# Performance work log

Hardware: AMD Instinct MI355X
Metric: run time of the kernel (lower is better)

## Reference

```python
import jax, jax.numpy as jnp
import numpy as np

B, L, D, H = 4, 2048, 1024, 16
DV = D // H


def setup_inputs() -> dict:
    key = jax.random.key(0)
    ks = jax.random.split(key, 11)
    s = 1.0 / np.sqrt(D)
    return {
        "query": jax.random.normal(ks[0], (B, L, D), jnp.float32),
        "key": jax.random.normal(ks[1], (B, L, D), jnp.float32),
        "value": jax.random.normal(ks[2], (B, L, D), jnp.float32),
        "Wq": jax.random.normal(ks[3], (D, D), jnp.float32) * s,
        "bq": jnp.zeros((D,), jnp.float32),
        "Wk": jax.random.normal(ks[4], (D, D), jnp.float32) * s,
        "bk": jnp.zeros((D,), jnp.float32),
        "Wv": jax.random.normal(ks[5], (D, D), jnp.float32) * s,
        "bv": jnp.zeros((D,), jnp.float32),
        "Wc": jax.random.normal(ks[6], (D, D), jnp.float32) * s,
        "bc": jnp.zeros((D,), jnp.float32),
    }


def _split(x):
    # [B, L, D] -> [B, H, L, DV]
    b, l, d = x.shape
    return x.reshape(b, l, H, DV).transpose(0, 2, 1, 3)


def reference(query, key, value, Wq, bq, Wk, bk, Wv, bv, Wc, bc):
    # Linear projections (torch Linear: x @ W.T + b)
    hq = _split(query @ Wq.T + bq)
    hk = _split(key @ Wk.T + bk)
    hv = _split(value @ Wv.T + bv)
    scale = 1.0 / jnp.sqrt(jnp.float32(DV))
    scores = jnp.einsum("bhqd,bhkd->bhqk", hq, hk) * scale  # [B,H,L,L]
    p = jax.nn.softmax(scores, axis=-1)
    out = jnp.einsum("bhqk,bhkd->bhqd", p, hv)  # [B,H,L,DV]
    out = out.transpose(0, 2, 1, 3).reshape(out.shape[0], out.shape[2], D)
    return out @ Wc.T + bc
```

## Files before the change

kernel.cpp:

```cpp
#include <hip/hip_runtime.h>

#define DI __device__ __forceinline__

typedef __attribute__((ext_vector_type(8))) short bf16x8;
typedef __attribute__((ext_vector_type(4))) float f32x4;
typedef __attribute__((ext_vector_type(16))) float f32x16;
typedef __attribute__((ext_vector_type(4))) unsigned u32x4;
typedef __attribute__((ext_vector_type(2))) unsigned u32x2;

static constexpr int B_ = 4, L_ = 2048, D_ = 1024, H_ = 16, DV_ = 64;
static constexpr int M_ = B_ * L_;
static constexpr float SCALE_LOG2 = 0.18033688011112042f;

DI short f2b(float f) {
  union { float f; unsigned u; } v; v.f = f;
  unsigned r = v.u + 0x7FFFu + ((v.u >> 16) & 1u);
  return (short)(r >> 16);
}

DI float b2f(short s) {
  union { unsigned u; float f; } v;
  v.u = ((unsigned)(unsigned short)s) << 16;
  return v.f;
}

DI unsigned cvtpk(float lo, float hi) {
  unsigned r;
  asm("v_cvt_pk_bf16_f32 %0, %1, %2" : "=v"(r) : "v"(lo), "v"(hi));
  return r;
}

DI void gl_lds16(const void* g, void* l) {
  __builtin_amdgcn_global_load_lds(
      (const __attribute__((address_space(1))) unsigned int*)g,
      (__attribute__((address_space(3))) unsigned int*)l, 16, 0, 0);
}

#define MFMA16(a, b, c) __builtin_amdgcn_mfma_f32_16x16x32_bf16((a), (b), (c), 0, 0, 0)
#define MFMA32(a, b, c) __builtin_amdgcn_mfma_f32_32x32x16_bf16((a), (b), (c), 0, 0, 0)

__global__ __launch_bounds__(256) void cvtw_kernel(const float* __restrict__ W0,
                                                   const float* __restrict__ W1,
                                                   const float* __restrict__ W2,
                                                   const float* __restrict__ W3,
                                                   short* __restrict__ dst) {
  const int p = blockIdx.y;
  const float* s = p == 0 ? W0 : p == 1 ? W1 : p == 2 ? W2 : W3;
  short* d = dst + (size_t)p * 1048576;
  int i0 = (blockIdx.x * 256 + threadIdx.x) * 8;
  int stride = gridDim.x * 256 * 8;
  for (int i = i0; i < 1048576; i += stride) {
    float4 a = *(const float4*)(s + i);
    float4 b = *(const float4*)(s + i + 4);
    u32x4 o;
    o[0] = cvtpk(a.x, a.y);
    o[1] = cvtpk(a.z, a.w);
    o[2] = cvtpk(b.x, b.y);
    o[3] = cvtpk(b.z, b.w);
    *(u32x4*)(d + i) = o;
  }
}

__global__ __launch_bounds__(256) void gemm_qkvf(const float* __restrict__ Xq,
                                                 const float* __restrict__ Xk,
                                                 const float* __restrict__ Xv,
                                                 const short* __restrict__ Wall,
                                                 const float* __restrict__ bq,
                                                 const float* __restrict__ bk,
                                                 const float* __restrict__ bv,
                                                 short* __restrict__ Hq,
                                                 short* __restrict__ Hk,
                                                 short* __restrict__ Hv) {
  constexpr int K = 1024, N = 1024;
  __shared__ __align__(16) float Asf[128 * 32];
  __shared__ __align__(16) short Bs[128 * 32];
  const int p = blockIdx.y;
  const float* A = p == 0 ? Xq : p == 1 ? Xk : Xv;
  const short* Wt = Wall + (size_t)p * 1048576;
  const float* bias = p == 0 ? bq : p == 1 ? bk : bv;
  short* outb = p == 0 ? Hq : p == 1 ? Hk : Hv;

  const int tid = threadIdx.x;
  const int w = tid >> 6, lane = tid & 63;
  const int c = lane & 15, g = lane >> 4;
  const int bid = (blockIdx.x & 7) * 64 + (blockIdx.x >> 3);
  const int bn = bid & 7, bm = bid >> 3;
  const int wr = w >> 1, wc = w & 1;

  f32x4 acc[4][4] = {};

  for (int kt = 0; kt < K / 32; ++kt) {
    __syncthreads();
#pragma unroll
    for (int it = 0; it < 4; ++it) {
      int slot = it * 256 + tid;
      int row = slot >> 3, ch = (slot & 7) ^ (row & 7);
      gl_lds16(A + ((size_t)(bm * 128 + row) * K + kt * 32 + ch * 4),
               &Asf[(it * 256 + w * 64) * 4]);
    }
#pragma unroll
    for (int ia = 0; ia < 2; ++ia) {
      int slot = ia * 256 + tid;
      int row = slot >> 2, ch = slot & 3;
      gl_lds16(Wt + ((size_t)(bn * 128 + row) * K + kt * 32 + ch * 8),
               &Bs[(ia * 256 + w * 64) * 8]);
    }
    __syncthreads();
    bf16x8 af[4], bf[4];
#pragma unroll
    for (int mi = 0; mi < 4; ++mi) {
      int r = wr * 64 + mi * 16 + c;
      int c0 = (((2 * g) ^ (r & 7)) * 4);
      int c1 = (((2 * g + 1) ^ (r & 7)) * 4);
      float4 lo = *(const float4*)&Asf[r * 32 + c0];
      float4 hi = *(const float4*)&Asf[r * 32 + c1];
      u32x4 pk;
      pk[0] = cvtpk(lo.x, lo.y);
      pk[1] = cvtpk(lo.z, lo.w);
      pk[2] = cvtpk(hi.x, hi.y);
      pk[3] = cvtpk(hi.z, hi.w);
      af[mi] = __builtin_bit_cast(bf16x8, pk);
    }
#pragma unroll
    for (int ni = 0; ni < 4; ++ni)
      bf[ni] = *(const bf16x8*)&Bs[(wc * 64 + ni * 16 + c) * 32 + g * 8];
#pragma unroll
    for (int mi = 0; mi < 4; ++mi)
#pragma unroll
      for (int ni = 0; ni < 4; ++ni)
        acc[mi][ni] = MFMA16(af[mi], bf[ni], acc[mi][ni]);
  }

  float bvv[4];
#pragma unroll
  for (int ni = 0; ni < 4; ++ni) bvv[ni] = bias[bn * 128 + wc * 64 + ni * 16 + c];
#pragma unroll
  for (int mi = 0; mi < 4; ++mi)
#pragma unroll
    for (int ni = 0; ni < 4; ++ni)
#pragma unroll
      for (int j = 0; j < 4; ++j) {
        int row = bm * 128 + wr * 64 + mi * 16 + g * 4 + j;
        int col = bn * 128 + wc * 64 + ni * 16 + c;
        outb[(size_t)row * N + col] = f2b(acc[mi][ni][j] + bvv[ni]);
      }
}

template <int OUTF32>
__global__ __launch_bounds__(256) void gemm_bt(const short* __restrict__ A,
                                               const short* __restrict__ Wt,
                                               const float* __restrict__ bias,
                                               float* __restrict__ outf,
                                               short* __restrict__ outb) {
  constexpr int K = 1024, N = 1024;
  __shared__ __align__(16) short As[128 * 32];
  __shared__ __align__(16) short Bs[128 * 32];
  const int tid = threadIdx.x;
  const int w = tid >> 6, lane = tid & 63;
  const int c = lane & 15, g = lane >> 4;
  const int bid = (blockIdx.x & 7) * 64 + (blockIdx.x >> 3);
  const int bn = bid & 7, bm = bid >> 3;
  const int wr = w >> 1, wc = w & 1;

  f32x4 acc[4][4] = {};

  for (int kt = 0; kt < K / 32; ++kt) {
    __syncthreads();
#pragma unroll
    for (int ia = 0; ia < 2; ++ia) {
      int slot = ia * 256 + tid;
      int row = slot >> 2, ch = slot & 3;
      gl_lds16(A + ((size_t)(bm * 128 + row) * K + kt * 32 + ch * 8),
               &As[(ia * 256 + w * 64) * 8]);
      gl_lds16(Wt + ((size_t)(bn * 128 + row) * K + kt * 32 + ch * 8),
               &Bs[(ia * 256 + w * 64) * 8]);
    }
    __syncthreads();
    bf16x8 af[4], bf[4];
#pragma unroll
    for (int mi = 0; mi < 4; ++mi)
      af[mi] = *(const bf16x8*)&As[(wr * 64 + mi * 16 + c) * 32 + g * 8];
#pragma unroll
    for (int ni = 0; ni < 4; ++ni)
      bf[ni] = *(const bf16x8*)&Bs[(wc * 64 + ni * 16 + c) * 32 + g * 8];
#pragma unroll
    for (int mi = 0; mi < 4; ++mi)
#pragma unroll
      for (int ni = 0; ni < 4; ++ni)
        acc[mi][ni] = MFMA16(af[mi], bf[ni], acc[mi][ni]);
  }

  float bv[4];
#pragma unroll
  for (int ni = 0; ni < 4; ++ni) bv[ni] = bias[bn * 128 + wc * 64 + ni * 16 + c];
#pragma unroll
  for (int mi = 0; mi < 4; ++mi)
#pragma unroll
    for (int ni = 0; ni < 4; ++ni)
#pragma unroll
      for (int j = 0; j < 4; ++j) {
        int row = bm * 128 + wr * 64 + mi * 16 + g * 4 + j;
        int col = bn * 128 + wc * 64 + ni * 16 + c;
        float v = acc[mi][ni][j] + bv[ni];
        if (OUTF32)
          outf[(size_t)row * N + col] = v;
        else
          outb[(size_t)row * N + col] = f2b(v);
      }
}

__global__ __launch_bounds__(256) void transpose_kernel(const short* __restrict__ Hv,
                                                        short* __restrict__ Hvt) {
  __shared__ short T[64 * 72];
  int bid = blockIdx.x;
  const int lt = bid & 31;
  const int h = (bid >> 5) & 15;
  const int b = bid >> 9;
  const int l0 = lt * 64;
  const int tid = threadIdx.x;
#pragma unroll
  for (int it = 0; it < 2; ++it) {
    int slot = it * 256 + tid;
    int r = slot >> 3, ch = slot & 7;
    bf16x8 v = *(const bf16x8*)&Hv[(size_t)(b * L_ + l0 + r) * D_ + h * DV_ + ch * 8];
    *(bf16x8*)&T[r * 72 + ch * 8] = v;
  }
  __syncthreads();
#pragma unroll
  for (int it = 0; it < 2; ++it) {
    int slot = it * 256 + tid;
    int dv = slot >> 3, ch = slot & 7;
    bf16x8 o;
#pragma unroll
    for (int i = 0; i < 8; ++i) o[i] = T[(ch * 8 + i) * 72 + dv];
    *(bf16x8*)&Hvt[(size_t)((b * H_ + h) * DV_ + dv) * L_ + l0 + ch * 8] = o;
  }
}

__global__ __launch_bounds__(256, 2) void attn_kernel(const short* __restrict__ Hq,
                                                      const short* __restrict__ Hk,
                                                      const short* __restrict__ Hvt,
                                                      short* __restrict__ Aout) {
  __shared__ __align__(16) short lds[34816];
  const int tid = threadIdx.x;
  const int w = tid >> 6, lane = tid & 63;
  const int c31 = lane & 31, g1 = lane >> 5;
  const int sw = (blockIdx.x & 7) * 64 + (blockIdx.x >> 3);
  const int qb = sw & 7;
  const int h = (sw >> 3) & 15;
  const int b = sw >> 7;
  const int q0 = qb * 256;

  bf16x8 qf0[4], qf1[4];
#pragma unroll
  for (int hh = 0; hh < 2; ++hh) {
    const short* qptr =
        Hq + (size_t)(b * L_ + q0 + w * 64 + hh * 32 + c31) * D_ + h * 64 + g1 * 8;
#pragma unroll
    for (int ks = 0; ks < 4; ++ks) {
      bf16x8 raw = *(const bf16x8*)(qptr + ks * 16);
      u32x4 pk;
#pragma unroll
      for (int i = 0; i < 4; ++i)
        pk[i] = cvtpk(b2f(raw[2 * i]) * SCALE_LOG2, b2f(raw[2 * i + 1]) * SCALE_LOG2);
      if (hh == 0) qf0[ks] = __builtin_bit_cast(bf16x8, pk);
      else         qf1[ks] = __builtin_bit_cast(bf16x8, pk);
    }
  }

  f32x16 O00 = {}, O01 = {}, O10 = {}, O11 = {};
  float ls0 = 0.f, ls1 = 0.f;
  unsigned* Pw0 = (unsigned*)(lds + 16384) + (w * 2 + 0) * 1152;
  unsigned* Pw1 = (unsigned*)(lds + 16384) + (w * 2 + 1) * 1152;

  auto stage = [&](int buf, int kv0) {
    short* Kb = lds + buf * 8192;
    short* Vb = Kb + 4096;
#pragma unroll
    for (int it = 0; it < 2; ++it) {
      int slot = it * 256 + tid;
      int row = slot >> 3;
      int ch = (slot & 7) ^ (row & 7);
      gl_lds16(Hk + (size_t)(b * L_ + kv0 + row) * D_ + h * 64 + ch * 8,
               Kb + (it * 256 + w * 64) * 8);
      gl_lds16(Hvt + (size_t)((b * H_ + h) * DV_ + row) * L_ + kv0 + ch * 8,
               Vb + (it * 256 + w * 64) * 8);
    }
  };

  stage(0, 0);
  int cur = 0;
  for (int t = 0; t < L_ / 64; ++t) {
    __syncthreads();
    if (t + 1 < L_ / 64) stage(cur ^ 1, (t + 1) * 64);
    const short* Kb = lds + cur * 8192;
    const short* Vb = Kb + 4096;

    f32x16 sA0 = {}, sB0 = {}, sA1 = {}, sB1 = {};
    __builtin_amdgcn_s_setprio(1);
#pragma unroll
    for (int ks = 0; ks < 4; ++ks) {
      int cp = (((2 * ks + g1) ^ (c31 & 7)) * 8);
      bf16x8 k0 = *(const bf16x8*)(Kb + c31 * 64 + cp);
      bf16x8 k1 = *(const bf16x8*)(Kb + (32 + c31) * 64 + cp);
      sA0 = MFMA32(k0, qf0[ks], sA0);
      sB0 = MFMA32(k1, qf0[ks], sB0);
      sA1 = MFMA32(k0, qf1[ks], sA1);
      sB1 = MFMA32(k1, qf1[ks], sB1);
    }
    __builtin_amdgcn_s_setprio(0);

    {
      float rs = 0.f;
#pragma unroll
      for (int p = 0; p < 4; ++p) {
        float a0 = __builtin_amdgcn_exp2f(sA0[4 * p]);
        float a1 = __builtin_amdgcn_exp2f(sA0[4 * p + 1]);
        float a2 = __builtin_amdgcn_exp2f(sA0[4 * p + 2]);
        float a3 = __builtin_amdgcn_exp2f(sA0[4 * p + 3]);
        float b0 = __builtin_amdgcn_exp2f(sB0[4 * p]);
        float b1 = __builtin_amdgcn_exp2f(sB0[4 * p + 1]);
        float b2 = __builtin_amdgcn_exp2f(sB0[4 * p + 2]);
        float b3 = __builtin_amdgcn_exp2f(sB0[4 * p + 3]);
        rs += (a0 + a1) + (a2 + a3) + (b0 + b1) + (b2 + b3);
        u32x2 lo, hi;
        lo[0] = cvtpk(a0, a1);
        lo[1] = cvtpk(a2, a3);
        hi[0] = cvtpk(b0, b1);
        hi[1] = cvtpk(b2, b3);
        *(u32x2*)(Pw0 + c31 * 36 + 4 * p + 2 * g1) = lo;
        *(u32x2*)(Pw0 + c31 * 36 + 16 + 4 * p + 2 * g1) = hi;
      }
      ls0 += rs + __shfl_xor(rs, 32);
    }
    {
      float rs = 0.f;
#pragma unroll
      for (int p = 0; p < 4; ++p) {
        float a0 = __builtin_amdgcn_exp2f(sA1[4 * p]);
        float a1 = __builtin_amdgcn_exp2f(sA1[4 * p + 1]);
        float a2 = __builtin_amdgcn_exp2f(sA1[4 * p + 2]);
        float a3 = __builtin_amdgcn_exp2f(sA1[4 * p + 3]);
        float b0 = __builtin_amdgcn_exp2f(sB1[4 * p]);
        float b1 = __builtin_amdgcn_exp2f(sB1[4 * p + 1]);
        float b2 = __builtin_amdgcn_exp2f(sB1[4 * p + 2]);
        float b3 = __builtin_amdgcn_exp2f(sB1[4 * p + 3]);
        rs += (a0 + a1) + (a2 + a3) + (b0 + b1) + (b2 + b3);
        u32x2 lo, hi;
        lo[0] = cvtpk(a0, a1);
        lo[1] = cvtpk(a2, a3);
        hi[0] = cvtpk(b0, b1);
        hi[1] = cvtpk(b2, b3);
        *(u32x2*)(Pw1 + c31 * 36 + 4 * p + 2 * g1) = lo;
        *(u32x2*)(Pw1 + c31 * 36 + 16 + 4 * p + 2 * g1) = hi;
      }
      ls1 += rs + __shfl_xor(rs, 32);
    }

    __builtin_amdgcn_s_setprio(1);
#pragma unroll
    for (int ks2 = 0; ks2 < 4; ++ks2) {
      int cp = (((2 * ks2 + g1) ^ (c31 & 7)) * 8);
      bf16x8 vf0 = *(const bf16x8*)(Vb + c31 * 64 + cp);
      bf16x8 vf1 = *(const bf16x8*)(Vb + (32 + c31) * 64 + cp);
      u32x4 pk0 = *(const u32x4*)(Pw0 + c31 * 36 + ks2 * 8 + g1 * 4);
      bf16x8 pf0 = __builtin_bit_cast(bf16x8, pk0);
      O00 = MFMA32(vf0, pf0, O00);
      O01 = MFMA32(vf1, pf0, O01);
      u32x4 pk1 = *(const u32x4*)(Pw1 + c31 * 36 + ks2 * 8 + g1 * 4);
      bf16x8 pf1 = __builtin_bit_cast(bf16x8, pk1);
      O10 = MFMA32(vf0, pf1, O10);
      O11 = MFMA32(vf1, pf1, O11);
    }
    __builtin_amdgcn_s_setprio(0);
    cur ^= 1;
  }

  float inv0 = 1.0f / ls0;
  float inv1 = 1.0f / ls1;
  __syncthreads();
  short* Os = lds;
#define EPI(OA, OB, INV, HH)                                        \
  {                                                                 \
    _Pragma("unroll") for (int dt = 0; dt < 2; ++dt) {              \
      _Pragma("unroll") for (int rq = 0; rq < 4; ++rq) {            \
        float e0 = (dt ? OB[4 * rq] : OA[4 * rq]) * INV;            \
        float e1 = (dt ? OB[4 * rq + 1] : OA[4 * rq + 1]) * INV;    \
        float e2 = (dt ? OB[4 * rq + 2] : OA[4 * rq + 2]) * INV;    \
        float e3 = (dt ? OB[4 * rq + 3] : OA[4 * rq + 3]) * INV;    \
        u32x2 pr;                                                   \
        pr[0] = cvtpk(e0, e1);                                      \
        pr[1] = cvtpk(e2, e3);                                      \
        int q = w * 64 + (HH)*32 + c31;                             \
        int dv = dt * 32 + 8 * rq + 4 * g1;                         \
        *(u32x2*)&Os[q * 72 + dv] = pr;                             \
      }                                                             \
    }                                                               \
  }
  EPI(O00, O01, inv0, 0)
  EPI(O10, O11, inv1, 1)
#undef EPI
  __syncthreads();
#pragma unroll
  for (int it = 0; it < 2; ++it) {
    const int r = it * 128 + (tid >> 1), hf = tid & 1;
    const size_t obase = (size_t)(b * L_ + q0 + r) * D_ + h * 64 + hf * 32;
#pragma unroll
    for (int cc = 0; cc < 4; ++cc) {
      bf16x8 vv = *(const bf16x8*)&Os[r * 72 + hf * 32 + cc * 8];
      *(bf16x8*)&Aout[obase + cc * 8] = vv;
    }
  }
}

extern "C" void kernel_launch(void* const* d_in, const int* in_sizes, int n_in,
                              void* d_out, int out_size, void* d_ws, size_t ws_size,
                              hipStream_t stream) {
  (void)in_sizes; (void)n_in; (void)out_size; (void)ws_size;
  const float* q = (const float*)d_in[0];
  const float* k = (const float*)d_in[1];
  const float* v = (const float*)d_in[2];
  const float* Wq = (const float*)d_in[3];
  const float* bq = (const float*)d_in[4];
  const float* Wk = (const float*)d_in[5];
  const float* bk = (const float*)d_in[6];
  const float* Wv = (const float*)d_in[7];
  const float* bv = (const float*)d_in[8];
  const float* Wc = (const float*)d_in[9];
  const float* bc = (const float*)d_in[10];
  float* out = (float*)d_out;

  short* ws = (short*)d_ws;
  const size_t SZ = (size_t)M_ * D_;
  const size_t WSZ = (size_t)D_ * D_;
  short* wqb = ws;
  short* wcb = ws + 3 * WSZ;
  short* hq = ws + 4 * WSZ;
  short* hk = hq + SZ;
  short* hv = hk + SZ;
  short* hvt = hv + SZ;
  short* aout = hv;

  dim3 gw(128, 4);
  cvtw_kernel<<<gw, 256, 0, stream>>>(Wq, Wk, Wv, Wc, wqb);

  dim3 gq(512, 3);
  gemm_qkvf<<<gq, 256, 0, stream>>>(q, k, v, wqb, bq, bk, bv, hq, hk, hv);

  transpose_kernel<<<2048, 256, 0, stream>>>(hv, hvt);

  attn_kernel<<<512, 256, 0, stream>>>(hq, hk, hvt, aout);

  gemm_bt<1><<<512, 256, 0, stream>>>(aout, wcb, bc, out, nullptr);
}
```

Baseline: 203.6 us.

## Widen QKV GEMM tile to 256 columns and fuse V transpose into epilogue

The QKV projection GEMM now computes a 128x256 output tile per block, with two B sub-tiles sharing each fp32 A tile. This halves the redundant global reads and bf16 conversions of the activation input. The V projection writes its output directly in the transposed per-head layout the attention kernel expects, so the separate transpose kernel and its round trip through memory are removed. In exchange, each block holds twice the accumulators, which raises register pressure, and the grid is halved. The transposed V stores are small strided 8-byte writes, which may coalesce poorly.

```diff
diff --git a/kernel.cpp b/kernel.cpp
--- a/kernel.cpp
+++ b/kernel.cpp
@@ -3,6 +3,7 @@
 #define DI __device__ __forceinline__
 
 typedef __attribute__((ext_vector_type(8))) short bf16x8;
+typedef __attribute__((ext_vector_type(4))) short bf16x4;
 typedef __attribute__((ext_vector_type(4))) float f32x4;
 typedef __attribute__((ext_vector_type(16))) float f32x16;
 typedef __attribute__((ext_vector_type(4))) unsigned u32x4;
@@ -61,33 +62,34 @@
   }
 }
 
-__global__ __launch_bounds__(256) void gemm_qkvf(const float* __restrict__ Xq,
-                                                 const float* __restrict__ Xk,
-                                                 const float* __restrict__ Xv,
-                                                 const short* __restrict__ Wall,
-                                                 const float* __restrict__ bq,
-                                                 const float* __restrict__ bk,
-                                                 const float* __restrict__ bv,
-                                                 short* __restrict__ Hq,
-                                                 short* __restrict__ Hk,
-                                                 short* __restrict__ Hv) {
+__global__ __launch_bounds__(256, 3) void gemm_qkvf(const float* __restrict__ Xq,
+                                                    const float* __restrict__ Xk,
+                                                    const float* __restrict__ Xv,
+                                                    const short* __restrict__ Wall,
+                                                    const float* __restrict__ bq,
+                                                    const float* __restrict__ bk,
+                                                    const float* __restrict__ bv,
+                                                    short* __restrict__ Hq,
+                                                    short* __restrict__ Hk,
+                                                    short* __restrict__ Hvt) {
   constexpr int K = 1024, N = 1024;
   __shared__ __align__(16) float Asf[128 * 32];
-  __shared__ __align__(16) short Bs[128 * 32];
+  __shared__ __align__(16) short Bs[2][128 * 32];
   const int p = blockIdx.y;
   const float* A = p == 0 ? Xq : p == 1 ? Xk : Xv;
   const short* Wt = Wall + (size_t)p * 1048576;
   const float* bias = p == 0 ? bq : p == 1 ? bk : bv;
-  short* outb = p == 0 ? Hq : p == 1 ? Hk : Hv;
+  short* outb = p == 0 ? Hq : p == 1 ? Hk : Hvt;
 
   const int tid = threadIdx.x;
   const int w = tid >> 6, lane = tid & 63;
   const int c = lane & 15, g = lane >> 4;
-  const int bid = (blockIdx.x & 7) * 64 + (blockIdx.x >> 3);
-  const int bn = bid & 7, bm = bid >> 3;
+  const int bid = (blockIdx.x & 7) * 32 + (blockIdx.x >> 3);
+  const int bn = bid & 3, bm = bid >> 2;
   const int wr = w >> 1, wc = w & 1;
 
-  f32x4 acc[4][4] = {};
+  f32x4 acc0[4][4] = {};
+  f32x4 acc1[4][4] = {};
 
   for (int kt = 0; kt < K / 32; ++kt) {
     __syncthreads();
@@ -99,14 +101,16 @@
                &Asf[(it * 256 + w * 64) * 4]);
     }
 #pragma unroll
-    for (int ia = 0; ia < 2; ++ia) {
-      int slot = ia * 256 + tid;
-      int row = slot >> 2, ch = slot & 3;
-      gl_lds16(Wt + ((size_t)(bn * 128 + row) * K + kt * 32 + ch * 8),
-               &Bs[(ia * 256 + w * 64) * 8]);
-    }
+    for (int bn2 = 0; bn2 < 2; ++bn2)
+#pragma unroll
+      for (int ia = 0; ia < 2; ++ia) {
+        int slot = ia * 256 + tid;
+        int row = slot >> 2, ch = slot & 3;
+        gl_lds16(Wt + ((size_t)(bn * 256 + bn2 * 128 + row) * K + kt * 32 + ch * 8),
+                 &Bs[bn2][(ia * 256 + w * 64) * 8]);
+      }
     __syncthreads();
-    bf16x8 af[4], bf[4];
+    bf16x8 af[4], bf0[4], bf1[4];
 #pragma unroll
     for (int mi = 0; mi < 4; ++mi) {
       int r = wr * 64 + mi * 16 + c;
@@ -122,28 +126,54 @@
       af[mi] = __builtin_bit_cast(bf16x8, pk);
     }
 #pragma unroll
+    for (int ni = 0; ni < 4; ++ni) {
+      bf0[ni] = *(const bf16x8*)&Bs[0][(wc * 64 + ni * 16 + c) * 32 + g * 8];
+      bf1[ni] = *(const bf16x8*)&Bs[1][(wc * 64 + ni * 16 + c) * 32 + g * 8];
+    }
+#pragma unroll
+    for (int mi = 0; mi < 4; ++mi)
+#pragma unroll
+      for (int ni = 0; ni < 4; ++ni) {
+        acc0[mi][ni] = MFMA16(af[mi], bf0[ni], acc0[mi][ni]);
+        acc1[mi][ni] = MFMA16(af[mi], bf1[ni], acc1[mi][ni]);
+      }
+  }
+
+#pragma unroll
+  for (int bn2 = 0; bn2 < 2; ++bn2) {
+    float bvv[4];
+#pragma unroll
     for (int ni = 0; ni < 4; ++ni)
-      bf[ni] = *(const bf16x8*)&Bs[(wc * 64 + ni * 16 + c) * 32 + g * 8];
-#pragma unroll
-    for (int mi = 0; mi < 4; ++mi)
-#pragma unroll
-      for (int ni = 0; ni < 4; ++ni)
-        acc[mi][ni] = MFMA16(af[mi], bf[ni], acc[mi][ni]);
-  }
-
-  float bvv[4];
-#pragma unroll
-  for (int ni = 0; ni < 4; ++ni) bvv[ni] = bias[bn * 128 + wc * 64 + ni * 16 + c];
-#pragma unroll
-  for (int mi = 0; mi < 4; ++mi)
-#pragma unroll
-    for (int ni = 0; ni < 4; ++ni)
-#pragma unroll
-      for (int j = 0; j < 4; ++j) {
-        int row = bm * 128 + wr * 64 + mi * 16 + g * 4 + j;
-        int col = bn * 128 + wc * 64 + ni * 16 + c;
-        outb[(size_t)row * N + col] = f2b(acc[mi][ni][j] + bvv[ni]);
-      }
+      bvv[ni] = bias[bn * 256 + bn2 * 128 + wc * 64 + ni * 16 + c];
+    if (p == 2) {
+#pragma unroll
+      for (int mi = 0; mi < 4; ++mi)
+#pragma unroll
+        for (int ni = 0; ni < 4; ++ni) {
+          int col = bn * 256 + bn2 * 128 + wc * 64 + ni * 16 + c;
+          int hh = col >> 6, dv = col & 63;
+          int row0 = bm * 128 + wr * 64 + mi * 16 + g * 4;
+          int bb = row0 >> 11, l0 = row0 & 2047;
+          f32x4 a = bn2 ? acc1[mi][ni] : acc0[mi][ni];
+          bf16x4 o;
+#pragma unroll
+          for (int j = 0; j < 4; ++j) o[j] = f2b(a[j] + bvv[ni]);
+          *(bf16x4*)&outb[((size_t)(bb * 16 + hh) * 64 + dv) * 2048 + l0] = o;
+        }
+    } else {
+#pragma unroll
+      for (int mi = 0; mi < 4; ++mi)
+#pragma unroll
+        for (int ni = 0; ni < 4; ++ni)
+#pragma unroll
+          for (int j = 0; j < 4; ++j) {
+            int row = bm * 128 + wr * 64 + mi * 16 + g * 4 + j;
+            int col = bn * 256 + bn2 * 128 + wc * 64 + ni * 16 + c;
+            f32x4 a = bn2 ? acc1[mi][ni] : acc0[mi][ni];
+            outb[(size_t)row * N + col] = f2b(a[j] + bvv[ni]);
+          }
+    }
+  }
 }
 
 template <int OUTF32>
@@ -207,34 +237,6 @@
         else
           outb[(size_t)row * N + col] = f2b(v);
       }
-}
-
-__global__ __launch_bounds__(256) void transpose_kernel(const short* __restrict__ Hv,
-                                                        short* __restrict__ Hvt) {
-  __shared__ short T[64 * 72];
-  int bid = blockIdx.x;
-  const int lt = bid & 31;
-  const int h = (bid >> 5) & 15;
-  const int b = bid >> 9;
-  const int l0 = lt * 64;
-  const int tid = threadIdx.x;
-#pragma unroll
-  for (int it = 0; it < 2; ++it) {
-    int slot = it * 256 + tid;
-    int r = slot >> 3, ch = slot & 7;
-    bf16x8 v = *(const bf16x8*)&Hv[(size_t)(b * L_ + l0 + r) * D_ + h * DV_ + ch * 8];
-    *(bf16x8*)&T[r * 72 + ch * 8] = v;
-  }
-  __syncthreads();
-#pragma unroll
-  for (int it = 0; it < 2; ++it) {
-    int slot = it * 256 + tid;
-    int dv = slot >> 3, ch = slot & 7;
-    bf16x8 o;
-#pragma unroll
-    for (int i = 0; i < 8; ++i) o[i] = T[(ch * 8 + i) * 72 + dv];
-    *(bf16x8*)&Hvt[(size_t)((b * H_ + h) * DV_ + dv) * L_ + l0 + ch * 8] = o;
-  }
 }
 
 __global__ __launch_bounds__(256, 2) void attn_kernel(const short* __restrict__ Hq,
@@ -437,17 +439,14 @@
   short* wcb = ws + 3 * WSZ;
   short* hq = ws + 4 * WSZ;
   short* hk = hq + SZ;
-  short* hv = hk + SZ;
-  short* hvt = hv + SZ;
-  short* aout = hv;
+  short* hvt = hk + SZ;
+  short* aout = hvt + SZ;
 
   dim3 gw(128, 4);
   cvtw_kernel<<<gw, 256, 0, stream>>>(Wq, Wk, Wv, Wc, wqb);
 
-  dim3 gq(512, 3);
-  gemm_qkvf<<<gq, 256, 0, stream>>>(q, k, v, wqb, bq, bk, bv, hq, hk, hv);
-
-  transpose_kernel<<<2048, 256, 0, stream>>>(hv, hvt);
+  dim3 gq(256, 3);
+  gemm_qkvf<<<gq, 256, 0, stream>>>(q, k, v, wqb, bq, bk, bv, hq, hk, hvt);
 
   attn_kernel<<<512, 256, 0, stream>>>(hq, hk, hvt, aout);
 
```

New measurement: 293.1 us. 44.0% more time.

## Widen QKV projection tile to 128x256 to reuse fp32 A conversion

Applied to the files above, without the earlier changes.

The fused QKV GEMM now computes a 128x256 output tile per block instead of 128x128, loading two B sub-tiles per k-step and keeping two accumulator sets. Each fp32 A tile is loaded and converted to bf16 once per 256 output columns, which halves the A global traffic and the conversion work. The grid shrinks to 256x3 blocks and the register footprint doubles, with launch bounds set to 3 waves/SIMD, so occupancy and spill risk trade against the reduced A reloads.

```diff
diff --git a/kernel.cpp b/kernel.cpp
--- a/kernel.cpp
+++ b/kernel.cpp
@@ -61,19 +61,19 @@
   }
 }
 
-__global__ __launch_bounds__(256) void gemm_qkvf(const float* __restrict__ Xq,
-                                                 const float* __restrict__ Xk,
-                                                 const float* __restrict__ Xv,
-                                                 const short* __restrict__ Wall,
-                                                 const float* __restrict__ bq,
-                                                 const float* __restrict__ bk,
-                                                 const float* __restrict__ bv,
-                                                 short* __restrict__ Hq,
-                                                 short* __restrict__ Hk,
-                                                 short* __restrict__ Hv) {
+__global__ __launch_bounds__(256, 3) void gemm_qkvf(const float* __restrict__ Xq,
+                                                    const float* __restrict__ Xk,
+                                                    const float* __restrict__ Xv,
+                                                    const short* __restrict__ Wall,
+                                                    const float* __restrict__ bq,
+                                                    const float* __restrict__ bk,
+                                                    const float* __restrict__ bv,
+                                                    short* __restrict__ Hq,
+                                                    short* __restrict__ Hk,
+                                                    short* __restrict__ Hv) {
   constexpr int K = 1024, N = 1024;
   __shared__ __align__(16) float Asf[128 * 32];
-  __shared__ __align__(16) short Bs[128 * 32];
+  __shared__ __align__(16) short Bs[2][128 * 32];
   const int p = blockIdx.y;
   const float* A = p == 0 ? Xq : p == 1 ? Xk : Xv;
   const short* Wt = Wall + (size_t)p * 1048576;
@@ -83,11 +83,12 @@
   const int tid = threadIdx.x;
   const int w = tid >> 6, lane = tid & 63;
   const int c = lane & 15, g = lane >> 4;
-  const int bid = (blockIdx.x & 7) * 64 + (blockIdx.x >> 3);
-  const int bn = bid & 7, bm = bid >> 3;
+  const int bid = (blockIdx.x & 7) * 32 + (blockIdx.x >> 3);
+  const int bn = bid & 3, bm = bid >> 2;
   const int wr = w >> 1, wc = w & 1;
 
-  f32x4 acc[4][4] = {};
+  f32x4 acc0[4][4] = {};
+  f32x4 acc1[4][4] = {};
 
   for (int kt = 0; kt < K / 32; ++kt) {
     __syncthreads();
@@ -99,14 +100,16 @@
                &Asf[(it * 256 + w * 64) * 4]);
     }
 #pragma unroll
-    for (int ia = 0; ia < 2; ++ia) {
-      int slot = ia * 256 + tid;
-      int row = slot >> 2, ch = slot & 3;
-      gl_lds16(Wt + ((size_t)(bn * 128 + row) * K + kt * 32 + ch * 8),
-               &Bs[(ia * 256 + w * 64) * 8]);
-    }
+    for (int bn2 = 0; bn2 < 2; ++bn2)
+#pragma unroll
+      for (int ia = 0; ia < 2; ++ia) {
+        int slot = ia * 256 + tid;
+        int row = slot >> 2, ch = slot & 3;
+        gl_lds16(Wt + ((size_t)(bn * 256 + bn2 * 128 + row) * K + kt * 32 + ch * 8),
+                 &Bs[bn2][(ia * 256 + w * 64) * 8]);
+      }
     __syncthreads();
-    bf16x8 af[4], bf[4];
+    bf16x8 af[4], bf0[4], bf1[4];
 #pragma unroll
     for (int mi = 0; mi < 4; ++mi) {
       int r = wr * 64 + mi * 16 + c;
@@ -122,28 +125,37 @@
       af[mi] = __builtin_bit_cast(bf16x8, pk);
     }
 #pragma unroll
+    for (int ni = 0; ni < 4; ++ni) {
+      bf0[ni] = *(const bf16x8*)&Bs[0][(wc * 64 + ni * 16 + c) * 32 + g * 8];
+      bf1[ni] = *(const bf16x8*)&Bs[1][(wc * 64 + ni * 16 + c) * 32 + g * 8];
+    }
+#pragma unroll
+    for (int mi = 0; mi < 4; ++mi)
+#pragma unroll
+      for (int ni = 0; ni < 4; ++ni) {
+        acc0[mi][ni] = MFMA16(af[mi], bf0[ni], acc0[mi][ni]);
+        acc1[mi][ni] = MFMA16(af[mi], bf1[ni], acc1[mi][ni]);
+      }
+  }
+
+#pragma unroll
+  for (int bn2 = 0; bn2 < 2; ++bn2) {
+    float bvv[4];
+#pragma unroll
     for (int ni = 0; ni < 4; ++ni)
-      bf[ni] = *(const bf16x8*)&Bs[(wc * 64 + ni * 16 + c) * 32 + g * 8];
+      bvv[ni] = bias[bn * 256 + bn2 * 128 + wc * 64 + ni * 16 + c];
 #pragma unroll
     for (int mi = 0; mi < 4; ++mi)
 #pragma unroll
       for (int ni = 0; ni < 4; ++ni)
-        acc[mi][ni] = MFMA16(af[mi], bf[ni], acc[mi][ni]);
-  }
-
-  float bvv[4];
-#pragma unroll
-  for (int ni = 0; ni < 4; ++ni) bvv[ni] = bias[bn * 128 + wc * 64 + ni * 16 + c];
-#pragma unroll
-  for (int mi = 0; mi < 4; ++mi)
-#pragma unroll
-    for (int ni = 0; ni < 4; ++ni)
-#pragma unroll
-      for (int j = 0; j < 4; ++j) {
-        int row = bm * 128 + wr * 64 + mi * 16 + g * 4 + j;
-        int col = bn * 128 + wc * 64 + ni * 16 + c;
-        outb[(size_t)row * N + col] = f2b(acc[mi][ni][j] + bvv[ni]);
-      }
+#pragma unroll
+        for (int j = 0; j < 4; ++j) {
+          int row = bm * 128 + wr * 64 + mi * 16 + g * 4 + j;
+          int col = bn * 256 + bn2 * 128 + wc * 64 + ni * 16 + c;
+          f32x4 a = bn2 ? acc1[mi][ni] : acc0[mi][ni];
+          outb[(size_t)row * N + col] = f2b(a[j] + bvv[ni]);
+        }
+  }
 }
 
 template <int OUTF32>
@@ -444,7 +456,7 @@
   dim3 gw(128, 4);
   cvtw_kernel<<<gw, 256, 0, stream>>>(Wq, Wk, Wv, Wc, wqb);
 
-  dim3 gq(512, 3);
+  dim3 gq(256, 3);
   gemm_qkvf<<<gq, 256, 0, stream>>>(q, k, v, wqb, bq, bk, bv, hq, hk, hv);
 
   transpose_kernel<<<2048, 256, 0, stream>>>(hv, hvt);
```

Measured after the change: 282.6 us. 1.39x slower.
